# Kernel optimization log

Hardware: AMD Instinct MI355X
Metric: run time of the kernel (lower is better)

## Reference

```python
import jax, jax.numpy as jnp
import numpy as np

B, L, D, K = 16, 2048, 128, 8192
NUM_RQ_STEPS = 1


def _nearest(residual, codebook):
    # residual: [B,L,D], codebook: [K,D]
    d2 = (
        jnp.sum(residual * residual, axis=-1, keepdims=True)  # [B,L,1]
        - 2.0 * jnp.einsum('bld,kd->blk', residual, codebook)  # [B,L,K]
        + jnp.sum(codebook * codebook, axis=-1)  # [K]
    )
    idx = jnp.argmin(d2, axis=-1)  # [B,L]
    return codebook[idx], idx  # gather: [B,L,D]


def setup_inputs() -> dict:
    key = jax.random.key(0)
    k1, k2 = jax.random.split(key)
    z_e = jax.random.normal(k1, (B, L, D), dtype=jnp.float32)
    codebook = jax.random.normal(k2, (K, D), dtype=jnp.float32)
    return {"z_e": z_e, "codebook": codebook}


def reference(z_e, codebook):
    # apply_codebook(z_e, code_sg=True): codebook is stop-gradiented,
    # residual quantization over NUM_RQ_STEPS, straight-through on output.
    cb = jax.lax.stop_gradient(codebook)
    residual = z_e
    z_q = jnp.zeros_like(z_e)
    idx_list = []
    for _ in range(NUM_RQ_STEPS):
        q, idx = _nearest(residual, cb)
        z_q = z_q + q
        residual = residual - q
        idx_list.append(idx)
    indices = jnp.stack(idx_list, axis=-1)  # [B,L,num_rq_steps]
    # straight-through estimator (code_sg=True): grads flow to z_e, not codebook
    z_q = z_e + jax.lax.stop_gradient(z_q - z_e)
    return z_q, indices
```

## Files before the change

kernel.cpp:

```cpp
#include <hip/hip_runtime.h>


#define M_TOK  32768
#define DIM    128
#define KCODES 8192
#define BM     64
#define NT     (KCODES / 256)
#define MARGIN 0.10f

typedef _Float16 half8v __attribute__((ext_vector_type(8)));
typedef float float4v __attribute__((ext_vector_type(4)));

union H2U { _Float16 h; unsigned short u; };
__device__ __forceinline__ unsigned short f2h_bits(_Float16 h) {
  H2U c; c.h = h; return c.u;
}

__device__ __forceinline__ void gload_lds16(const void* g, void* l) {
  __builtin_amdgcn_global_load_lds(
      (const __attribute__((address_space(1))) unsigned int*)g,
      (__attribute__((address_space(3))) unsigned int*)l, 16, 0, 0);
}

#define CNORM_OFF  (KCODES * 256)
#define QCNT_OFF   (CNORM_OFF + KCODES * 4)
#define QTOK_OFF   (QCNT_OFF + 64)
#define KMIN_OFF   (QTOK_OFF + M_TOK * 4)

__global__ __launch_bounds__(256) void prep_kernel(
    const float* __restrict__ cb, unsigned short* __restrict__ Cs,
    float* __restrict__ cnorm, int* __restrict__ qcnt) {
  if (blockIdx.x == 0 && threadIdx.x == 0) *qcnt = 0;
  const int k = blockIdx.x * 4 + (threadIdx.x >> 6);
  const int lane = threadIdx.x & 63;
  const float2 v = ((const float2*)(cb + (size_t)k * DIM))[lane];
  float s = v.x * v.x + v.y * v.y;
  #pragma unroll
  for (int off = 32; off > 0; off >>= 1) s += __shfl_down(s, off);
  if (lane == 0) cnorm[k] = s;
  ushort2 hi;
  hi.x = f2h_bits((_Float16)v.x);
  hi.y = f2h_bits((_Float16)v.y);
  *(ushort2*)(Cs + (size_t)k * 128 + lane * 2) = hi;
}

__global__ __launch_bounds__(256, 2) void vq_mfma_kernel(
    const float* __restrict__ ze, const unsigned short* __restrict__ Cs,
    const float* __restrict__ cnorm, const float* __restrict__ cb,
    int* __restrict__ qcnt, int* __restrict__ qtok,
    unsigned long long* __restrict__ kmin,
    float* __restrict__ out_zq, float* __restrict__ out_idx) {
  __shared__ char lds[49152];
  char* const As = lds;
  char* const Bs = lds + 16384;

  const int tid = threadIdx.x;
  const int wn = tid >> 6;
  const int lane = tid & 63;
  const int quad = lane >> 4;
  const int l15 = lane & 15;
  const int m0 = blockIdx.x * BM;

  int loffC[4];
  #pragma unroll
  for (int c = 0; c < 4; ++c) {
    const int r = c * 16 + (lane >> 2);
    const int s = lane & 3;
    const int seg = s ^ ((r >> 1) & 3);
    loffC[c] = (wn * 64 + r) * 256 + seg * 16;
  }
  int boff[4];
  #pragma unroll
  for (int j = 0; j < 4; ++j) {
    const int n = j * 16 + l15;
    boff[j] = n * 64 + ((quad ^ ((n >> 1) & 3)) << 4);
  }
  char* const BsW = Bs + wn * 8192;

  {
    const int r = tid >> 2;
    const int qh = tid & 3;
    const float* zrow = ze + (size_t)(m0 + r) * DIM + qh * 32;
    char* arow = As + r * 256;
    const int rx = r & 7;
    #pragma unroll
    for (int i = 0; i < 8; ++i) {
      const float4 v = *(const float4*)(zrow + i * 4);
      ushort4 hh;
      hh.x = f2h_bits((_Float16)v.x);
      hh.y = f2h_bits((_Float16)v.y);
      hh.z = f2h_bits((_Float16)v.z);
      hh.w = f2h_bits((_Float16)v.w);
      const int c = qh * 32 + i * 4;
      *(ushort4*)(arow + ((((c >> 3) ^ rx) << 4) | ((c & 7) << 1))) = hh;
    }
  }
  __syncthreads();

  half8v ahi[4][4];
  #pragma unroll
  for (int ks = 0; ks < 4; ++ks)
    #pragma unroll
    for (int i = 0; i < 4; ++i) {
      const int m = i * 16 + l15;
      const int kslot = ks * 4 + quad;
      ahi[ks][i] = *(const half8v*)(As + m * 256 + ((kslot ^ (m & 7)) << 4));
    }

  float bestv[16], secv[16], idxv[16];
  #pragma unroll
  for (int s = 0; s < 16; ++s) {
    bestv[s] = -3.4e38f; secv[s] = -3.4e38f; idxv[s] = 0.f;
  }

  for (int nt = 0; nt < NT; ++nt) {
    const char* const tile = (const char*)Cs + (size_t)nt * 65536;
    float cnv[4];
    #pragma unroll
    for (int j = 0; j < 4; ++j)
      cnv[j] = cnorm[nt * 256 + wn * 64 + j * 16 + l15];

    float4v acc[4][4];
    #pragma unroll
    for (int j = 0; j < 4; ++j) {
      const float b = -0.5f * cnv[j];
      #pragma unroll
      for (int i = 0; i < 4; ++i) {
        acc[i][j][0] = b; acc[i][j][1] = b;
        acc[i][j][2] = b; acc[i][j][3] = b;
      }
    }

    #pragma unroll
    for (int t = 0; t < 2; ++t) {
      __syncthreads();
      #pragma unroll
      for (int p = 0; p < 2; ++p)
        #pragma unroll
        for (int c = 0; c < 4; ++c)
          gload_lds16(tile + (t * 2 + p) * 64 + loffC[c],
                      BsW + p * 4096 + c * 1024);
      __syncthreads();

      #pragma unroll
      for (int p = 0; p < 2; ++p) {
        const int kk = t * 2 + p;
        half8v bf[4];
        #pragma unroll
        for (int j = 0; j < 4; ++j)
          bf[j] = *(const half8v*)(BsW + p * 4096 + boff[j]);
        #pragma unroll
        for (int i = 0; i < 4; ++i)
          #pragma unroll
          for (int j = 0; j < 4; ++j)
            acc[i][j] = __builtin_amdgcn_mfma_f32_16x16x32_f16(
                ahi[kk][i], bf[j], acc[i][j], 0, 0, 0);
      }
    }

    #pragma unroll
    for (int j = 0; j < 4; ++j) {
      const float nidx = (float)(nt * 256 + wn * 64 + j * 16 + l15);
      #pragma unroll
      for (int i = 0; i < 4; ++i)
        #pragma unroll
        for (int rg = 0; rg < 4; ++rg) {
          const float sc = acc[i][j][rg];
          const int slot = i * 4 + rg;
          const bool bt = sc > bestv[slot];
          secv[slot] = __builtin_amdgcn_fmed3f(sc, bestv[slot], secv[slot]);
          idxv[slot] = bt ? nidx : idxv[slot];
          bestv[slot] = fmaxf(bestv[slot], sc);
        }
    }
  }

  #pragma unroll
  for (int slot = 0; slot < 16; ++slot) {
    float b = bestv[slot], sec = secv[slot], ix = idxv[slot];
    #pragma unroll
    for (int mk = 1; mk <= 8; mk <<= 1) {
      const float ob = __shfl_xor(b, mk);
      const float os = __shfl_xor(sec, mk);
      const float oi = __shfl_xor(ix, mk);
      const bool take = (ob > b) || (ob == b && oi < ix);
      const float loser = take ? b : ob;
      b = take ? ob : b;
      ix = take ? oi : ix;
      sec = fmaxf(fmaxf(sec, os), loser);
    }
    bestv[slot] = b; secv[slot] = sec; idxv[slot] = ix;
  }

  __syncthreads();
  float* const redB = (float*)lds;
  float* const redS = redB + 256;
  float* const redI = redB + 512;
  float* const lidxs = redB + 768;
  if (l15 == 0) {
    #pragma unroll
    for (int slot = 0; slot < 16; ++slot) {
      const int row = (slot >> 2) * 16 + quad * 4 + (slot & 3);
      redB[wn * 64 + row] = bestv[slot];
      redS[wn * 64 + row] = secv[slot];
      redI[wn * 64 + row] = idxv[slot];
    }
  }
  __syncthreads();
  if (tid < 64) {
    float b = redB[tid], sec = redS[tid], ix = redI[tid];
    #pragma unroll
    for (int w = 1; w < 4; ++w) {
      const float ob = redB[w * 64 + tid];
      const float os = redS[w * 64 + tid];
      const float oi = redI[w * 64 + tid];
      const bool take = (ob > b) || (ob == b && oi < ix);
      const float loser = take ? b : ob;
      b = take ? ob : b;
      ix = take ? oi : ix;
      sec = fmaxf(fmaxf(sec, os), loser);
    }
    out_idx[m0 + tid] = ix;
    lidxs[tid] = ix;
    if (b - sec < 0.5f * MARGIN) {
      kmin[m0 + tid] = ~0ull;
      const int p = atomicAdd(qcnt, 1);
      qtok[p] = m0 + tid;
    }
  }
  __syncthreads();

  const int tl = tid >> 2, qp = tid & 3;
  const int code = (int)lidxs[tl];
  const float4* src = (const float4*)(cb + (size_t)code * DIM);
  float4* dst = (float4*)(out_zq + (size_t)(m0 + tl) * DIM);
  #pragma unroll
  for (int p = 0; p < 8; ++p) dst[qp + p * 4] = src[qp + p * 4];
}

__global__ __launch_bounds__(256) void rescan_part_kernel(
    const float* __restrict__ ze, const float* __restrict__ cb,
    const float* __restrict__ cnorm, const int* __restrict__ qcnt,
    const int* __restrict__ qtok, unsigned long long* __restrict__ kmin) {
  __shared__ float xsh[DIM];
  __shared__ float rs[256];
  __shared__ int ri[256];
  const int tid = threadIdx.x;
  const int chunk = blockIdx.x & 31;
  const int n = *qcnt;
  for (int qi = blockIdx.x >> 5; qi < n; qi += (gridDim.x >> 5)) {
    const int token = qtok[qi];
    __syncthreads();
    if (tid < 32)
      ((float4*)xsh)[tid] = ((const float4*)(ze + (size_t)token * DIM))[tid];
    __syncthreads();
    const int code = chunk * 256 + tid;
    const float* crow = cb + (size_t)code * DIM;
    float dot = 0.f;
    #pragma unroll
    for (int d = 0; d < DIM; ++d) dot = fmaf(xsh[d], crow[d], dot);
    rs[tid] = fmaf(-2.f, dot, cnorm[code]);
    ri[tid] = code;
    __syncthreads();
    #pragma unroll
    for (int off = 128; off > 0; off >>= 1) {
      if (tid < off) {
        const float so = rs[tid + off];
        const int io = ri[tid + off];
        if (so < rs[tid] || (so == rs[tid] && io < ri[tid])) {
          rs[tid] = so; ri[tid] = io;
        }
      }
      __syncthreads();
    }
    if (tid == 0) {
      union { float f; unsigned int u; } c; c.f = rs[0];
      const unsigned int m = (c.u >> 31) ? ~c.u : (c.u | 0x80000000u);
      const unsigned long long key =
          ((unsigned long long)m << 32) | (unsigned int)ri[0];
      atomicMin(&kmin[token], key);
    }
    __syncthreads();
  }
}

__global__ __launch_bounds__(256) void rescan_apply_kernel(
    const float* __restrict__ cb, const int* __restrict__ qcnt,
    const int* __restrict__ qtok, const unsigned long long* __restrict__ kmin,
    float* __restrict__ out_zq, float* __restrict__ out_idx) {
  const int tid = threadIdx.x;
  const int n = *qcnt;
  for (int qi = blockIdx.x; qi < n; qi += gridDim.x) {
    const int token = qtok[qi];
    const int code = (int)(unsigned int)(kmin[token] & 0xFFFFFFFFull);
    if (tid == 0) out_idx[token] = (float)code;
    if (tid < 32)
      ((float4*)(out_zq + (size_t)token * DIM))[tid] =
          ((const float4*)(cb + (size_t)code * DIM))[tid];
  }
}

extern "C" void kernel_launch(void* const* d_in, const int* in_sizes, int n_in,
                              void* d_out, int out_size, void* d_ws,
                              size_t ws_size, hipStream_t stream) {
  const float* ze = (const float*)d_in[0];
  const float* cb = (const float*)d_in[1];
  float* out = (float*)d_out;

  unsigned short* Cs = (unsigned short*)d_ws;
  float* cnorm = (float*)((char*)d_ws + CNORM_OFF);
  int* qcnt = (int*)((char*)d_ws + QCNT_OFF);
  int* qtok = (int*)((char*)d_ws + QTOK_OFF);
  unsigned long long* kmin = (unsigned long long*)((char*)d_ws + KMIN_OFF);

  prep_kernel<<<KCODES / 4, 256, 0, stream>>>(cb, Cs, cnorm, qcnt);
  vq_mfma_kernel<<<M_TOK / BM, 256, 0, stream>>>(
      ze, Cs, cnorm, cb, qcnt, qtok, kmin, out, out + (size_t)M_TOK * DIM);
  rescan_part_kernel<<<4096, 256, 0, stream>>>(ze, cb, cnorm, qcnt, qtok,
                                               kmin);
  rescan_apply_kernel<<<256, 256, 0, stream>>>(cb, qcnt, qtok, kmin, out,
                                               out + (size_t)M_TOK * DIM);
}
```

Measured before the change: 281.1 us.

## Load codebook fragments directly from global into registers with double buffering

Drops the LDS staging of codebook tiles, along with the two block barriers per half-tile. Each wave now reads its MFMA B fragments straight from global/L2 into registers, double-buffered so the next k-slice loads while the current one is consumed. The cnorm bias moves from accumulator initialisation into the epilogue as an fma. This removes barrier stalls and shrinks LDS, but makes every wave fetch uncoalesced 16-byte pieces from global memory and relies on cache hits and latency hiding with only one slice of lookahead.

```diff
diff --git a/kernel.cpp b/kernel.cpp
--- a/kernel.cpp
+++ b/kernel.cpp
@@ -16,11 +16,17 @@
   H2U c; c.h = h; return c.u;
 }
 
-__device__ __forceinline__ void gload_lds16(const void* g, void* l) {
-  __builtin_amdgcn_global_load_lds(
-      (const __attribute__((address_space(1))) unsigned int*)g,
-      (__attribute__((address_space(3))) unsigned int*)l, 16, 0, 0);
-}
+#define LOADB(bf, base_off) do {                                     \
+    _Pragma("unroll") for (int j_ = 0; j_ < 4; ++j_)                 \
+      (bf)[j_] = *(const half8v*)(Bp[j_] + (base_off));              \
+  } while (0)
+
+#define CONSUME(kk, bf) do {                                         \
+    _Pragma("unroll") for (int i_ = 0; i_ < 4; ++i_)                 \
+      _Pragma("unroll") for (int j_ = 0; j_ < 4; ++j_)               \
+        acc[i_][j_] = __builtin_amdgcn_mfma_f32_16x16x32_f16(        \
+            ahi[kk][i_], (bf)[j_], acc[i_][j_], 0, 0, 0);            \
+  } while (0)
 
 #define CNORM_OFF  (KCODES * 256)
 #define QCNT_OFF   (CNORM_OFF + KCODES * 4)
@@ -50,9 +56,8 @@
     int* __restrict__ qcnt, int* __restrict__ qtok,
     unsigned long long* __restrict__ kmin,
     float* __restrict__ out_zq, float* __restrict__ out_idx) {
-  __shared__ char lds[49152];
+  __shared__ char lds[16384];
   char* const As = lds;
-  char* const Bs = lds + 16384;
 
   const int tid = threadIdx.x;
   const int wn = tid >> 6;
@@ -61,21 +66,11 @@
   const int l15 = lane & 15;
   const int m0 = blockIdx.x * BM;
 
-  int loffC[4];
-  #pragma unroll
-  for (int c = 0; c < 4; ++c) {
-    const int r = c * 16 + (lane >> 2);
-    const int s = lane & 3;
-    const int seg = s ^ ((r >> 1) & 3);
-    loffC[c] = (wn * 64 + r) * 256 + seg * 16;
-  }
-  int boff[4];
-  #pragma unroll
-  for (int j = 0; j < 4; ++j) {
-    const int n = j * 16 + l15;
-    boff[j] = n * 64 + ((quad ^ ((n >> 1) & 3)) << 4);
-  }
-  char* const BsW = Bs + wn * 8192;
+  const char* Bp[4];
+  #pragma unroll
+  for (int j = 0; j < 4; ++j)
+    Bp[j] = (const char*)Cs +
+            (size_t)(wn * 64 + j * 16 + l15) * 256 + quad * 16;
 
   {
     const int r = tid >> 2;
@@ -113,8 +108,11 @@
     bestv[s] = -3.4e38f; secv[s] = -3.4e38f; idxv[s] = 0.f;
   }
 
+  half8v bf0[4], bf1[4];
+  LOADB(bf0, 0);
+
   for (int nt = 0; nt < NT; ++nt) {
-    const char* const tile = (const char*)Cs + (size_t)nt * 65536;
+    const size_t tb = (size_t)nt * 65536;
     float cnv[4];
     #pragma unroll
     for (int j = 0; j < 4; ++j)
@@ -122,50 +120,28 @@
 
     float4v acc[4][4];
     #pragma unroll
-    for (int j = 0; j < 4; ++j) {
-      const float b = -0.5f * cnv[j];
+    for (int i = 0; i < 4; ++i)
       #pragma unroll
-      for (int i = 0; i < 4; ++i) {
-        acc[i][j][0] = b; acc[i][j][1] = b;
-        acc[i][j][2] = b; acc[i][j][3] = b;
-      }
-    }
-
-    #pragma unroll
-    for (int t = 0; t < 2; ++t) {
-      __syncthreads();
-      #pragma unroll
-      for (int p = 0; p < 2; ++p)
-        #pragma unroll
-        for (int c = 0; c < 4; ++c)
-          gload_lds16(tile + (t * 2 + p) * 64 + loffC[c],
-                      BsW + p * 4096 + c * 1024);
-      __syncthreads();
-
-      #pragma unroll
-      for (int p = 0; p < 2; ++p) {
-        const int kk = t * 2 + p;
-        half8v bf[4];
-        #pragma unroll
-        for (int j = 0; j < 4; ++j)
-          bf[j] = *(const half8v*)(BsW + p * 4096 + boff[j]);
-        #pragma unroll
-        for (int i = 0; i < 4; ++i)
-          #pragma unroll
-          for (int j = 0; j < 4; ++j)
-            acc[i][j] = __builtin_amdgcn_mfma_f32_16x16x32_f16(
-                ahi[kk][i], bf[j], acc[i][j], 0, 0, 0);
-      }
-    }
+      for (int j = 0; j < 4; ++j) acc[i][j] = (float4v)0.0f;
+
+    LOADB(bf1, tb + 1 * 64);
+    CONSUME(0, bf0);
+    LOADB(bf0, tb + 2 * 64);
+    CONSUME(1, bf1);
+    LOADB(bf1, tb + 3 * 64);
+    CONSUME(2, bf0);
+    if (nt + 1 < NT) LOADB(bf0, tb + 65536);
+    CONSUME(3, bf1);
 
     #pragma unroll
     for (int j = 0; j < 4; ++j) {
       const float nidx = (float)(nt * 256 + wn * 64 + j * 16 + l15);
+      const float cn = cnv[j];
       #pragma unroll
       for (int i = 0; i < 4; ++i)
         #pragma unroll
         for (int rg = 0; rg < 4; ++rg) {
-          const float sc = acc[i][j][rg];
+          const float sc = fmaf(-0.5f, cn, acc[i][j][rg]);
           const int slot = i * 4 + rg;
           const bool bt = sc > bestv[slot];
           secv[slot] = __builtin_amdgcn_fmed3f(sc, bestv[slot], secv[slot]);
```

Result: slower. 295.9 us (+5.3%).
